# Performance work log

Measured on AMD Instinct MI355X. Metric: run time of the kernel, lower is better.

Reference implementation:

```python
import jax, jax.numpy as jnp
import numpy as np

NUM_LABELS = 26
INPUT_DIM = 128
BATCH = 8192
WORD_LEN = 20


def setup_inputs() -> dict:
    key = jax.random.key(0)
    kx, kw, kt, ky = jax.random.split(key, 4)
    X = jax.random.normal(kx, (BATCH, WORD_LEN, INPUT_DIM), jnp.float32)
    Y = jax.random.randint(ky, (BATCH, WORD_LEN), 0, NUM_LABELS, dtype=jnp.int32)
    W = jax.random.normal(kw, (NUM_LABELS, INPUT_DIM), jnp.float32)
    T = jax.random.normal(kt, (NUM_LABELS, NUM_LABELS), jnp.float32)
    return {"X": X, "Y": Y, "W": W, "T": T}


def _crf_nll(X, Y, W, T):
    # Emission scores: emis[b, s, k] = W[k] . X[b, s]   -> [B, M, K]
    emis = jnp.einsum('bmd,kd->bmk', X, W)
    B, M, K = emis.shape

    # Forward (log-sum-exp) recursion over time, matching forward():
    #   alpha[i, j] = logsumexp_k( W[k].X[i-1] + T[k, j] + alpha[i-1, k] )
    def step(alpha, e_prev):
        # alpha: [B, K]; e_prev: [B, K]
        s = e_prev[:, :, None] + T[None, :, :] + alpha[:, :, None]  # [B, K_prev, K_cur]
        return jax.nn.logsumexp(s, axis=1), None

    alpha0 = jnp.zeros((B, K), X.dtype)
    # scan over the first M-1 emission timesteps (time-major)
    alpha_last, _ = jax.lax.scan(step, alpha0, jnp.moveaxis(emis[:, :-1, :], 1, 0))

    # log Z = logsumexp_k( W[k].X[m-1] + alpha[m-1, k] )
    log_z = jax.nn.logsumexp(emis[:, -1, :] + alpha_last, axis=-1)  # [B]

    # Node potential: sum_s W[y_s] . X[s]
    node = jnp.take_along_axis(emis, Y[:, :, None].astype(jnp.int32), axis=2)[:, :, 0].sum(axis=1)
    # Edge potential: sum_s T[y_s, y_{s+1}]
    edge = T[Y[:, :-1], Y[:, 1:]].sum(axis=1)

    # Negative log-likelihood summed over the batch
    return -(node + edge - log_z).sum()


def reference(X, Y, W, T):
    return _crf_nll(X, Y, W, T)
```

## Files before the change

### kernel.cpp

```cpp
#include <hip/hip_runtime.h>


typedef float f32x4 __attribute__((ext_vector_type(4)));
typedef __bf16 bf16x8 __attribute__((ext_vector_type(8)));
typedef unsigned int u32x4 __attribute__((ext_vector_type(4)));
typedef unsigned int u32x2 __attribute__((ext_vector_type(2)));

#define C_SCALE 1.4426950408889634f
#define LN2 0.6931471805599453f
#define NEGF (-3.0e38f)

__device__ __forceinline__ unsigned short f2bf(float f) {
    unsigned u = __float_as_uint(f);
    u += 0x7fffu + ((u >> 16) & 1u);
    return (unsigned short)(u >> 16);
}

__device__ __forceinline__ float lo16f(unsigned u) { return __uint_as_float(u << 16); }
__device__ __forceinline__ float hi16f(unsigned u) { return __uint_as_float(u & 0xFFFF0000u); }

__device__ __forceinline__ float qmax(float x) {
    float y = fmaxf(x, __shfl_xor(x, 16, 64));
    u32x2 r = __builtin_amdgcn_permlane32_swap(__float_as_uint(y), __float_as_uint(y), false, false);
    return fmaxf(__uint_as_float(r[0]), __uint_as_float(r[1]));
}
__device__ __forceinline__ float qsum(float x) {
    float y = x + __shfl_xor(x, 16, 64);
    u32x2 r = __builtin_amdgcn_permlane32_swap(__float_as_uint(y), __float_as_uint(y), false, false);
    return __uint_as_float(r[0]) + __uint_as_float(r[1]);
}

union ABu { unsigned int w[4]; bf16x8 b; unsigned short u[8]; };

__device__ __forceinline__ bf16x8 pack_bf8(f32x4 a, f32x4 b) {
    ABu r;
    r.u[0] = f2bf(a[0]); r.u[1] = f2bf(a[1]); r.u[2] = f2bf(a[2]); r.u[3] = f2bf(a[3]);
    r.u[4] = f2bf(b[0]); r.u[5] = f2bf(b[1]); r.u[6] = f2bf(b[2]); r.u[7] = f2bf(b[3]);
    return r.b;
}

__global__ __launch_bounds__(256, 2) void crf_kernel(
    const float* __restrict__ X, const int* __restrict__ Y,
    const float* __restrict__ W, const float* __restrict__ T,
    float* __restrict__ part)
{
    __shared__ unsigned e_lds[320 * 20];
    __shared__ float t_lds[26 * 26];
    __shared__ float red1;

    const int tid = threadIdx.x;
    const int w   = tid >> 6;
    const int l   = tid & 63;
    const int c0  = l & 15, kg = l >> 4;

    for (int i = tid; i < 676; i += 256) t_lds[i] = T[i];

    {
        ABu bfrag[4][2];
        const int koff = kg * 8;
        #pragma unroll
        for (int kk = 0; kk < 4; ++kk) {
            #pragma unroll
            for (int nt = 0; nt < 2; ++nt) {
                const int col = nt * 16 + c0;
                ABu f;
                if (col < 26) {
                    const float* wp = W + col * 128 + kk * 32 + koff;
                    f32x4 w0 = *(const f32x4*)wp;
                    f32x4 w1 = *(const f32x4*)(wp + 4);
                    f.b = pack_bf8(w0, w1);
                } else {
                    f.w[0] = f.w[1] = f.w[2] = f.w[3] = 0u;
                }
                bfrag[kk][nt] = f;
            }
        }
        const int rbase = w * 80;
        for (int t = 0; t < 5; ++t) {
            const float* xp = X + ((long)blockIdx.x * 320 + rbase + t * 16 + c0) * 128 + kg * 8;
            f32x4 acc0 = {0.f,0.f,0.f,0.f}, acc1 = {0.f,0.f,0.f,0.f};
            #pragma unroll
            for (int kk = 0; kk < 4; ++kk) {
                f32x4 x0 = *(const f32x4*)(xp + kk * 32);
                f32x4 x1 = *(const f32x4*)(xp + kk * 32 + 4);
                bf16x8 a = pack_bf8(x0, x1);
                acc0 = __builtin_amdgcn_mfma_f32_16x16x32_bf16(a, bfrag[kk][0].b, acc0, 0, 0, 0);
                acc1 = __builtin_amdgcn_mfma_f32_16x16x32_bf16(a, bfrag[kk][1].b, acc1, 0, 0, 0);
            }
            #pragma unroll
            for (int i = 0; i < 4; ++i) {
                const int rr = rbase + t * 16 + kg * 4 + i;
                const unsigned wlo = f2bf(acc0[i] * C_SCALE);
                const unsigned whi = f2bf(acc1[i] * C_SCALE);
                e_lds[rr * 20 + c0] = (whi << 16) | wlo;
            }
        }
    }
    __syncthreads();

    const int g = l >> 4, c = l & 15;
    const int elem = blockIdx.x * 16 + c;

    float myv = 0.f;

    if (w == 1) {
        const int ebase = elem * 20;
        float nd2 = 0.f, edn = 0.f;
        int y[6];
        #pragma unroll
        for (int t = 0; t < 5; ++t) y[t] = Y[ebase + 5 * g + t];
        y[5] = (g < 3) ? Y[ebase + 5 * g + 5] : 0;
        #pragma unroll
        for (int t = 0; t < 5; ++t) {
            const int m = 5 * g + t;
            const unsigned wv = e_lds[(c * 20 + m) * 20 + (y[t] & 15)];
            nd2 += (y[t] < 16) ? lo16f(wv) : hi16f(wv);
            if (m < 19) edn += t_lds[y[t] * 26 + y[t + 1]];
        }
        float v = -LN2 * nd2 - edn;
        #pragma unroll
        for (int d = 1; d <= 32; d <<= 1) v += __shfl_xor(v, d, 64);
        if (l == 0) red1 = v;
    }

    if (w == 0) {
        ABu A0, A1;
        #pragma unroll
        for (int jj = 0; jj < 8; ++jj) {
            const int kp = 4 * g + (jj & 3) + ((jj >> 2) << 4);
            float v0 = 0.f, v1 = 0.f;
            if (kp < 26) {
                v0 = __builtin_amdgcn_exp2f(t_lds[kp * 26 + c] * C_SCALE);
                if (16 + c < 26) v1 = __builtin_amdgcn_exp2f(t_lds[kp * 26 + 16 + c] * C_SCALE);
            }
            A0.u[jj] = f2bf(v0);
            A1.u[jj] = f2bf(v1);
        }

        u32x4 ev[20];
        #pragma unroll
        for (int m = 0; m < 20; ++m)
            ev[m] = *(const u32x4*)&e_lds[c * 400 + m * 20 + 4 * g];

        f32x4 s0, s1;
        #pragma unroll
        for (int i = 0; i < 4; ++i) { s0[i] = lo16f(ev[0][i]); s1[i] = hi16f(ev[0][i]); }
        if (16 + 4 * g + 0 >= 26) s1[0] = NEGF;
        if (16 + 4 * g + 1 >= 26) s1[1] = NEGF;
        if (16 + 4 * g + 2 >= 26) s1[2] = NEGF;
        if (16 + 4 * g + 3 >= 26) s1[3] = NEGF;

        const f32x4 z = {0.f, 0.f, 0.f, 0.f};
        #pragma unroll
        for (int m = 0; m < 19; ++m) {
            const float mx8 = fmaxf(fmaxf(fmaxf(s0[0], s0[1]), fmaxf(s0[2], s0[3])),
                                    fmaxf(fmaxf(s1[0], s1[1]), fmaxf(s1[2], s1[3])));
            const float mx = qmax(mx8);
            ABu B;
            B.u[0] = f2bf(__builtin_amdgcn_exp2f(s0[0] - mx));
            B.u[1] = f2bf(__builtin_amdgcn_exp2f(s0[1] - mx));
            B.u[2] = f2bf(__builtin_amdgcn_exp2f(s0[2] - mx));
            B.u[3] = f2bf(__builtin_amdgcn_exp2f(s0[3] - mx));
            B.u[4] = f2bf(__builtin_amdgcn_exp2f(s1[0] - mx));
            B.u[5] = f2bf(__builtin_amdgcn_exp2f(s1[1] - mx));
            B.u[6] = f2bf(__builtin_amdgcn_exp2f(s1[2] - mx));
            B.u[7] = f2bf(__builtin_amdgcn_exp2f(s1[3] - mx));
            f32x4 D0 = __builtin_amdgcn_mfma_f32_16x16x32_bf16(A0.b, B.b, z, 0, 0, 0);
            f32x4 D1 = __builtin_amdgcn_mfma_f32_16x16x32_bf16(A1.b, B.b, z, 0, 0, 0);
            #pragma unroll
            for (int i = 0; i < 4; ++i) {
                s0[i] = mx + __builtin_amdgcn_logf(D0[i]) + lo16f(ev[m + 1][i]);
                s1[i] = mx + __builtin_amdgcn_logf(D1[i]) + hi16f(ev[m + 1][i]);
            }
        }

        const float mxl = fmaxf(fmaxf(fmaxf(s0[0], s0[1]), fmaxf(s0[2], s0[3])),
                                fmaxf(fmaxf(s1[0], s1[1]), fmaxf(s1[2], s1[3])));
        const float mx2 = qmax(mxl);
        float sm = __builtin_amdgcn_exp2f(s0[0] - mx2) + __builtin_amdgcn_exp2f(s0[1] - mx2)
                 + __builtin_amdgcn_exp2f(s0[2] - mx2) + __builtin_amdgcn_exp2f(s0[3] - mx2)
                 + __builtin_amdgcn_exp2f(s1[0] - mx2) + __builtin_amdgcn_exp2f(s1[1] - mx2)
                 + __builtin_amdgcn_exp2f(s1[2] - mx2) + __builtin_amdgcn_exp2f(s1[3] - mx2);
        sm = qsum(sm);
        const float logZ2 = mx2 + __builtin_amdgcn_logf(sm);

        float v = (g == 0) ? LN2 * logZ2 : 0.f;
        #pragma unroll
        for (int d = 1; d <= 32; d <<= 1) v += __shfl_xor(v, d, 64);
        myv = v;
    }

    __syncthreads();

    if (w == 0 && l == 0) part[blockIdx.x] = myv + red1;
}

__global__ __launch_bounds__(256) void reduce_kernel(
    const float* __restrict__ part, float* __restrict__ out, int n)
{
    __shared__ float s[4];
    const int tid = threadIdx.x;
    float v = part[tid] + part[tid + 256];
    #pragma unroll
    for (int d = 1; d <= 32; d <<= 1) v += __shfl_xor(v, d, 64);
    if ((tid & 63) == 0) s[tid >> 6] = v;
    __syncthreads();
    if (tid == 0) out[0] = s[0] + s[1] + s[2] + s[3];
}

extern "C" void kernel_launch(void* const* d_in, const int* in_sizes, int n_in,
                              void* d_out, int out_size, void* d_ws, size_t ws_size,
                              hipStream_t stream) {
    const float* X = (const float*)d_in[0];
    const int*   Y = (const int*)d_in[1];
    const float* W = (const float*)d_in[2];
    const float* T = (const float*)d_in[3];
    float* out = (float*)d_out;
    float* part = (float*)d_ws;

    const int B = in_sizes[1] / 20;
    const int nblocks = B / 16;

    crf_kernel<<<nblocks, 256, 0, stream>>>(X, Y, W, T, part);
    reduce_kernel<<<1, 256, 0, stream>>>(part, out, nblocks);
}
```

Before: 30.23 us.

## Split CRF forward recursion across all waves and drop block barriers

Previously one wave ran the log-sum-exp recursion for all 16 sequences of a block while a second wave computed node and edge potentials, and two waves sat idle after the emission GEMM. Now each wave runs the recursion on the 4 sequences whose emissions it produced itself, replicating them across MFMA columns, and also computes their node and edge terms. Each wave then writes its own partial sum. This removes both __syncthreads and the T staging in LDS, and the reduce kernel is generalised to sum 4x as many partials. The cost is redundant MFMA and transcendental work on the replicated columns, plus T being read directly from global memory.

Result: slower. 35.68 us (+18.0%).

```diff
diff --git a/kernel.cpp b/kernel.cpp
--- a/kernel.cpp
+++ b/kernel.cpp
@@ -45,15 +45,11 @@
     float* __restrict__ part)
 {
     __shared__ unsigned e_lds[320 * 20];
-    __shared__ float t_lds[26 * 26];
-    __shared__ float red1;
 
     const int tid = threadIdx.x;
     const int w   = tid >> 6;
     const int l   = tid & 63;
     const int c0  = l & 15, kg = l >> 4;
-
-    for (int i = tid; i < 676; i += 256) t_lds[i] = T[i];
 
     {
         ABu bfrag[4][2];
@@ -96,103 +92,91 @@
             }
         }
     }
-    __syncthreads();
 
     const int g = l >> 4, c = l & 15;
-    const int elem = blockIdx.x * 16 + c;
-
-    float myv = 0.f;
-
-    if (w == 1) {
-        const int ebase = elem * 20;
+    const int ce = c & 3;
+
+    ABu A0, A1;
+    #pragma unroll
+    for (int jj = 0; jj < 8; ++jj) {
+        const int kp = 4 * g + (jj & 3) + ((jj >> 2) << 4);
+        float v0 = 0.f, v1 = 0.f;
+        if (kp < 26) {
+            v0 = __builtin_amdgcn_exp2f(T[kp * 26 + c] * C_SCALE);
+            if (16 + c < 26) v1 = __builtin_amdgcn_exp2f(T[kp * 26 + 16 + c] * C_SCALE);
+        }
+        A0.u[jj] = f2bf(v0);
+        A1.u[jj] = f2bf(v1);
+    }
+
+    u32x4 ev[20];
+    #pragma unroll
+    for (int m = 0; m < 20; ++m)
+        ev[m] = *(const u32x4*)&e_lds[(w * 80 + ce * 20 + m) * 20 + 4 * g];
+
+    f32x4 s0, s1;
+    #pragma unroll
+    for (int i = 0; i < 4; ++i) { s0[i] = lo16f(ev[0][i]); s1[i] = hi16f(ev[0][i]); }
+    if (16 + 4 * g + 0 >= 26) s1[0] = NEGF;
+    if (16 + 4 * g + 1 >= 26) s1[1] = NEGF;
+    if (16 + 4 * g + 2 >= 26) s1[2] = NEGF;
+    if (16 + 4 * g + 3 >= 26) s1[3] = NEGF;
+
+    const f32x4 z = {0.f, 0.f, 0.f, 0.f};
+    #pragma unroll
+    for (int m = 0; m < 19; ++m) {
+        const float mx8 = fmaxf(fmaxf(fmaxf(s0[0], s0[1]), fmaxf(s0[2], s0[3])),
+                                fmaxf(fmaxf(s1[0], s1[1]), fmaxf(s1[2], s1[3])));
+        const float mx = qmax(mx8);
+        ABu B;
+        B.u[0] = f2bf(__builtin_amdgcn_exp2f(s0[0] - mx));
+        B.u[1] = f2bf(__builtin_amdgcn_exp2f(s0[1] - mx));
+        B.u[2] = f2bf(__builtin_amdgcn_exp2f(s0[2] - mx));
+        B.u[3] = f2bf(__builtin_amdgcn_exp2f(s0[3] - mx));
+        B.u[4] = f2bf(__builtin_amdgcn_exp2f(s1[0] - mx));
+        B.u[5] = f2bf(__builtin_amdgcn_exp2f(s1[1] - mx));
+        B.u[6] = f2bf(__builtin_amdgcn_exp2f(s1[2] - mx));
+        B.u[7] = f2bf(__builtin_amdgcn_exp2f(s1[3] - mx));
+        f32x4 D0 = __builtin_amdgcn_mfma_f32_16x16x32_bf16(A0.b, B.b, z, 0, 0, 0);
+        f32x4 D1 = __builtin_amdgcn_mfma_f32_16x16x32_bf16(A1.b, B.b, z, 0, 0, 0);
+        #pragma unroll
+        for (int i = 0; i < 4; ++i) {
+            s0[i] = mx + __builtin_amdgcn_logf(D0[i]) + lo16f(ev[m + 1][i]);
+            s1[i] = mx + __builtin_amdgcn_logf(D1[i]) + hi16f(ev[m + 1][i]);
+        }
+    }
+
+    const float mxl = fmaxf(fmaxf(fmaxf(s0[0], s0[1]), fmaxf(s0[2], s0[3])),
+                            fmaxf(fmaxf(s1[0], s1[1]), fmaxf(s1[2], s1[3])));
+    const float mx2 = qmax(mxl);
+    float sm = __builtin_amdgcn_exp2f(s0[0] - mx2) + __builtin_amdgcn_exp2f(s0[1] - mx2)
+             + __builtin_amdgcn_exp2f(s0[2] - mx2) + __builtin_amdgcn_exp2f(s0[3] - mx2)
+             + __builtin_amdgcn_exp2f(s1[0] - mx2) + __builtin_amdgcn_exp2f(s1[1] - mx2)
+             + __builtin_amdgcn_exp2f(s1[2] - mx2) + __builtin_amdgcn_exp2f(s1[3] - mx2);
+    sm = qsum(sm);
+    const float logZ2 = mx2 + __builtin_amdgcn_logf(sm);
+
+    float v = 0.f;
+    if (c < 4) {
+        const int eglob = blockIdx.x * 16 + 4 * w + c;
         float nd2 = 0.f, edn = 0.f;
         int y[6];
         #pragma unroll
-        for (int t = 0; t < 5; ++t) y[t] = Y[ebase + 5 * g + t];
-        y[5] = (g < 3) ? Y[ebase + 5 * g + 5] : 0;
+        for (int t = 0; t < 5; ++t) y[t] = Y[eglob * 20 + 5 * g + t];
+        y[5] = (g < 3) ? Y[eglob * 20 + 5 * g + 5] : 0;
         #pragma unroll
         for (int t = 0; t < 5; ++t) {
             const int m = 5 * g + t;
-            const unsigned wv = e_lds[(c * 20 + m) * 20 + (y[t] & 15)];
+            const unsigned wv = e_lds[(w * 80 + c * 20 + m) * 20 + (y[t] & 15)];
             nd2 += (y[t] < 16) ? lo16f(wv) : hi16f(wv);
-            if (m < 19) edn += t_lds[y[t] * 26 + y[t + 1]];
-        }
-        float v = -LN2 * nd2 - edn;
-        #pragma unroll
-        for (int d = 1; d <= 32; d <<= 1) v += __shfl_xor(v, d, 64);
-        if (l == 0) red1 = v;
-    }
-
-    if (w == 0) {
-        ABu A0, A1;
-        #pragma unroll
-        for (int jj = 0; jj < 8; ++jj) {
-            const int kp = 4 * g + (jj & 3) + ((jj >> 2) << 4);
-            float v0 = 0.f, v1 = 0.f;
-            if (kp < 26) {
-                v0 = __builtin_amdgcn_exp2f(t_lds[kp * 26 + c] * C_SCALE);
-                if (16 + c < 26) v1 = __builtin_amdgcn_exp2f(t_lds[kp * 26 + 16 + c] * C_SCALE);
-            }
-            A0.u[jj] = f2bf(v0);
-            A1.u[jj] = f2bf(v1);
-        }
-
-        u32x4 ev[20];
-        #pragma unroll
-        for (int m = 0; m < 20; ++m)
-            ev[m] = *(const u32x4*)&e_lds[c * 400 + m * 20 + 4 * g];
-
-        f32x4 s0, s1;
-        #pragma unroll
-        for (int i = 0; i < 4; ++i) { s0[i] = lo16f(ev[0][i]); s1[i] = hi16f(ev[0][i]); }
-        if (16 + 4 * g + 0 >= 26) s1[0] = NEGF;
-        if (16 + 4 * g + 1 >= 26) s1[1] = NEGF;
-        if (16 + 4 * g + 2 >= 26) s1[2] = NEGF;
-        if (16 + 4 * g + 3 >= 26) s1[3] = NEGF;
-
-        const f32x4 z = {0.f, 0.f, 0.f, 0.f};
-        #pragma unroll
-        for (int m = 0; m < 19; ++m) {
-            const float mx8 = fmaxf(fmaxf(fmaxf(s0[0], s0[1]), fmaxf(s0[2], s0[3])),
-                                    fmaxf(fmaxf(s1[0], s1[1]), fmaxf(s1[2], s1[3])));
-            const float mx = qmax(mx8);
-            ABu B;
-            B.u[0] = f2bf(__builtin_amdgcn_exp2f(s0[0] - mx));
-            B.u[1] = f2bf(__builtin_amdgcn_exp2f(s0[1] - mx));
-            B.u[2] = f2bf(__builtin_amdgcn_exp2f(s0[2] - mx));
-            B.u[3] = f2bf(__builtin_amdgcn_exp2f(s0[3] - mx));
-            B.u[4] = f2bf(__builtin_amdgcn_exp2f(s1[0] - mx));
-            B.u[5] = f2bf(__builtin_amdgcn_exp2f(s1[1] - mx));
-            B.u[6] = f2bf(__builtin_amdgcn_exp2f(s1[2] - mx));
-            B.u[7] = f2bf(__builtin_amdgcn_exp2f(s1[3] - mx));
-            f32x4 D0 = __builtin_amdgcn_mfma_f32_16x16x32_bf16(A0.b, B.b, z, 0, 0, 0);
-            f32x4 D1 = __builtin_amdgcn_mfma_f32_16x16x32_bf16(A1.b, B.b, z, 0, 0, 0);
-            #pragma unroll
-            for (int i = 0; i < 4; ++i) {
-                s0[i] = mx + __builtin_amdgcn_logf(D0[i]) + lo16f(ev[m + 1][i]);
-                s1[i] = mx + __builtin_amdgcn_logf(D1[i]) + hi16f(ev[m + 1][i]);
-            }
-        }
-
-        const float mxl = fmaxf(fmaxf(fmaxf(s0[0], s0[1]), fmaxf(s0[2], s0[3])),
-                                fmaxf(fmaxf(s1[0], s1[1]), fmaxf(s1[2], s1[3])));
-        const float mx2 = qmax(mxl);
-        float sm = __builtin_amdgcn_exp2f(s0[0] - mx2) + __builtin_amdgcn_exp2f(s0[1] - mx2)
-                 + __builtin_amdgcn_exp2f(s0[2] - mx2) + __builtin_amdgcn_exp2f(s0[3] - mx2)
-                 + __builtin_amdgcn_exp2f(s1[0] - mx2) + __builtin_amdgcn_exp2f(s1[1] - mx2)
-                 + __builtin_amdgcn_exp2f(s1[2] - mx2) + __builtin_amdgcn_exp2f(s1[3] - mx2);
-        sm = qsum(sm);
-        const float logZ2 = mx2 + __builtin_amdgcn_logf(sm);
-
-        float v = (g == 0) ? LN2 * logZ2 : 0.f;
-        #pragma unroll
-        for (int d = 1; d <= 32; d <<= 1) v += __shfl_xor(v, d, 64);
-        myv = v;
-    }
-
-    __syncthreads();
-
-    if (w == 0 && l == 0) part[blockIdx.x] = myv + red1;
+            if (m < 19) edn += T[y[t] * 26 + y[t + 1]];
+        }
+        v = -LN2 * nd2 - edn;
+        if (g == 0) v += LN2 * logZ2;
+    }
+    #pragma unroll
+    for (int d = 1; d <= 32; d <<= 1) v += __shfl_xor(v, d, 64);
+    if (l == 0) part[blockIdx.x * 4 + w] = v;
 }
 
 __global__ __launch_bounds__(256) void reduce_kernel(
@@ -200,7 +184,8 @@
 {
     __shared__ float s[4];
     const int tid = threadIdx.x;
-    float v = part[tid] + part[tid + 256];
+    float v = 0.f;
+    for (int i = tid; i < n; i += 256) v += part[i];
     #pragma unroll
     for (int d = 1; d <= 32; d <<= 1) v += __shfl_xor(v, d, 64);
     if ((tid & 63) == 0) s[tid >> 6] = v;
@@ -222,5 +207,5 @@
     const int nblocks = B / 16;
 
     crf_kernel<<<nblocks, 256, 0, stream>>>(X, Y, W, T, part);
-    reduce_kernel<<<1, 256, 0, stream>>>(part, out, nblocks);
-}
+    reduce_kernel<<<1, 256, 0, stream>>>(part, out, nblocks * 4);
+}
```
